# Optimization experiments

Measured on AMD Instinct MI355X. Metric: run time of the kernel, lower is better.

The kernel has to match this reference:

```python
import jax, jax.numpy as jnp
import numpy as np

N_NEIGHBORS = 9
MIN_STD, MAX_STD = 0.01, 0.5
EPS_NORM = 1e-8


def setup_inputs() -> dict:
    key = jax.random.key(0)
    k1, k2, k3 = jax.random.split(key, 3)
    B, C, H, W = 8, 1024, 28, 28
    M, D = 16384, 1024
    features = jax.random.normal(k1, (B, C, H, W), dtype=jnp.float32)
    memory_bank = jax.random.normal(k2, (M, D), dtype=jnp.float32)
    influence_weight = jnp.ones((D,), dtype=jnp.float32)
    distance_weight = jnp.ones((1,), dtype=jnp.float32)
    eps = jax.random.normal(k3, (B * H * W, D), dtype=jnp.float32)  # randn_like noise
    return {"features": features, "memory_bank": memory_bank,
            "influence_weight": influence_weight, "distance_weight": distance_weight,
            "eps": eps}


def reference(features, memory_bank, influence_weight, distance_weight, eps):
    B, C, H, W = features.shape
    M, D = memory_bank.shape
    x = features.transpose(0, 2, 3, 1).reshape(B * H * W, C)  # [N, D]
    N = x.shape[0]

    d2 = (jnp.sum(x * x, axis=1, keepdims=True)
          + jnp.sum(memory_bank * memory_bank, axis=1)[None, :]
          - 2.0 * (x @ memory_bank.T))  # [N, M]
    dist = jnp.sqrt(jnp.clip(d2, 1e-12))

    k = min(N_NEIGHBORS, M)
    neg_topd, idx = jax.lax.top_k(-dist, k)  # smallest-k distances
    topk_distances = -neg_topd  # [N, k]

    # Per-dimension influence: mean |x - nn| over k neighbors, scaled by weight
    nn_feats = memory_bank[idx]  # [N, k, D] gather
    influence = jnp.abs(x[:, None, :] - nn_feats).mean(axis=1) * influence_weight[None, :]  # [N, D]

    # Row-wise normalization (torch std is unbiased, ddof=1)
    infl_norm = ((influence - influence.mean(axis=-1, keepdims=True))
                 / (jnp.std(influence, axis=-1, ddof=1, keepdims=True) + EPS_NORM))

    # Distance signal: per-row mean distance, normalized by global stats of the
    # [N, D]-expanded tensor (each row value repeated D times -> same mean,
    # unbiased std uses N*D - 1 in the denominator).
    ds = topk_distances.mean(axis=-1, keepdims=True)  # [N, 1]
    full_mean = ds.mean()
    full_std = jnp.sqrt(jnp.sum((ds - full_mean) ** 2) * D / (N * D - 1))
    dist_norm = (ds - full_mean) / (full_std + EPS_NORM)  # [N, 1], broadcasts over D

    combined = infl_norm + distance_weight * dist_norm  # [N, D]
    noise_std = MIN_STD + (MAX_STD - MIN_STD) * jax.nn.sigmoid(combined)

    noised = (x + eps * noise_std).reshape(B, H, W, C).transpose(0, 3, 1, 2)
    influence_map = influence.mean(axis=-1).reshape(B, H, W)
    noise_std_map = noise_std.mean(axis=-1).reshape(B, H, W)
    return noised, influence_map, noise_std_map
```

## Files before the change

kernel.cpp:

```cpp
#include <hip/hip_runtime.h>
#include <hip/hip_bf16.h>
#include <stdint.h>

#define N_ROWS 6272
#define DIM    1024
#define M_ROWS 16384
#define KNN    9
#define BMS    128
#define BNS    128
#define NPANEL 128
#define TOPC   6
#define NCAND  (NPANEL * 2 * TOPC)
#define TRR    16

typedef __attribute__((ext_vector_type(4))) float f32x4;
typedef __attribute__((ext_vector_type(4))) int   i32x4;
typedef __attribute__((ext_vector_type(16))) int  i32x16;

#define QSCALE 31.75f

__device__ __forceinline__ void async16(const void* g, void* l) {
  __builtin_amdgcn_global_load_lds(
      (const __attribute__((address_space(1))) unsigned int*)g,
      (__attribute__((address_space(3))) unsigned int*)l, 16, 0, 0);
}

__device__ __forceinline__ int quant8(float v) {
  return __float2int_rn(fminf(fmaxf(v, -4.f), 4.f) * QSCALE);
}

__device__ __forceinline__ int kswz(int row, int col) {
  return col ^ ((row & 7) << 2) ^ (((row >> 3) & 1) << 5);
}

__global__ void k_prep_x(const float* __restrict__ feat,
                         float* __restrict__ xf, signed char* __restrict__ xq) {
  const int n = blockIdx.x;
  const int b = n / 784, hw = n % 784;
  const float* src = feat + (size_t)b * (1024 * 784) + hw;
  float* xrow = xf + (size_t)n * DIM;
  signed char* qrow = xq + (size_t)n * DIM;
  for (int c = threadIdx.x; c < DIM; c += 256) {
    float v = src[(size_t)c * 784];
    xrow[c] = v;
    qrow[c] = (signed char)quant8(v);
  }
}

__global__ void k_prep_m(const float* __restrict__ mb,
                         signed char* __restrict__ mq, int* __restrict__ mni) {
  const int j = blockIdx.x;
  const int t = threadIdx.x;
  const float* src = mb + (size_t)j * DIM;
  signed char* dst = mq + (size_t)j * DIM;
  int s = 0;
  for (int c = t; c < DIM; c += 256) {
    const int q = quant8(src[c]);
    dst[c] = (signed char)q;
    s += q * q;
  }
  __shared__ int red[4];
#pragma unroll
  for (int o = 32; o >= 1; o >>= 1) s += __shfl_down(s, o);
  if ((t & 63) == 0) red[t >> 6] = s;
  __syncthreads();
  if (t == 0) mni[j] = red[0] + red[1] + red[2] + red[3];
}

__launch_bounds__(256, 2)
__global__ void k_score(const signed char* __restrict__ xq,
                        const signed char* __restrict__ mq,
                        const int* __restrict__ mni,
                        unsigned int* __restrict__ cand, int jhalf) {
  __shared__ signed char S[65536];
  __shared__ int mns[BNS];
  int* Kbuf = (int*)S;

  const int bx = blockIdx.x;
  const int xcd = bx & 7, i = bx >> 3;
  const int panel = i & 7, agroup = i >> 3;
  const int j0 = jhalf * 8192 + xcd * 1024 + panel * BNS;
  const int pglob = jhalf * 64 + xcd * 8 + panel;

  const int t = threadIdx.x;
  const int lane = t & 63, w = t >> 6;
  const int wr = w >> 1, wc = w & 1;
  const int l31 = lane & 31, kh = lane >> 5;

  int offL[4], aOff[4];
  const signed char* bP[4];
#pragma unroll
  for (int cpy = 0; cpy < 4; ++cpy) {
    const int off = cpy * 4096 + t * 16;
    const int row = off >> 7;
    const int col = (off & 127) ^ ((row & 7) << 4);
    offL[cpy] = off;
    aOff[cpy] = row * DIM + col;
    bP[cpy] = mq + (size_t)(j0 + row) * DIM + col;
  }
  if (t < BNS) mns[t] = mni[j0 + t];

#pragma unroll 1
  for (int k7 = 0; k7 < 7; ++k7) {
    const int tile = agroup + 7 * k7;
    const int r0 = tile * BMS;
    const signed char* aT = xq + (size_t)r0 * DIM;

    i32x16 acc[2][2];
#pragma unroll
    for (int mi = 0; mi < 2; ++mi)
#pragma unroll
      for (int ni = 0; ni < 2; ++ni)
#pragma unroll
        for (int r = 0; r < 16; ++r) acc[mi][ni][r] = 0;

#pragma unroll
    for (int cpy = 0; cpy < 4; ++cpy) {
      async16(aT + aOff[cpy], S + offL[cpy]);
      async16(bP[cpy], S + 32768 + offL[cpy]);
    }
#pragma unroll 1
    for (int kt = 0; kt < 8; ++kt) {
      if (kt < 7) {
        const int kk = (kt + 1) * 128;
        const int nb = ((kt + 1) & 1) * 16384;
#pragma unroll
        for (int cpy = 0; cpy < 4; ++cpy) {
          async16(aT + aOff[cpy] + kk, S + nb + offL[cpy]);
          async16(bP[cpy] + kk, S + 32768 + nb + offL[cpy]);
        }
        asm volatile("s_waitcnt vmcnt(8)" ::: "memory");
      } else {
        asm volatile("s_waitcnt vmcnt(0)" ::: "memory");
      }
      __builtin_amdgcn_s_barrier();
      const signed char* Ab = S + (kt & 1) * 16384;
      const signed char* Bb = S + 32768 + (kt & 1) * 16384;
      __builtin_amdgcn_s_setprio(1);
#pragma unroll
      for (int ks = 0; ks < 4; ++ks) {
        const int kcol = ks * 32 + kh * 16;
        i32x4 a[2], b[2];
#pragma unroll
        for (int mi = 0; mi < 2; ++mi) {
          const int row = wr * 64 + mi * 32 + l31;
          a[mi] = *(const i32x4*)(Ab + row * 128 + (kcol ^ ((row & 7) << 4)));
        }
#pragma unroll
        for (int ni = 0; ni < 2; ++ni) {
          const int row = wc * 64 + ni * 32 + l31;
          b[ni] = *(const i32x4*)(Bb + row * 128 + (kcol ^ ((row & 7) << 4)));
        }
#pragma unroll
        for (int mi = 0; mi < 2; ++mi)
#pragma unroll
          for (int ni = 0; ni < 2; ++ni)
            acc[mi][ni] = __builtin_amdgcn_mfma_i32_32x32x32_i8(a[mi], b[ni], acc[mi][ni], 0, 0, 0);
      }
      __builtin_amdgcn_s_setprio(0);
      asm volatile("" ::: "memory");
      __builtin_amdgcn_s_barrier();
    }

#pragma unroll
    for (int mi = 0; mi < 2; ++mi)
#pragma unroll
      for (int ni = 0; ni < 2; ++ni) {
        const int col = wc * 64 + ni * 32 + l31;
        const int mn = mns[col];
#pragma unroll
        for (int r = 0; r < 16; ++r) {
          const int row = wr * 64 + mi * 32 + 4 * kh + (r & 3) + 8 * (r >> 2);
          Kbuf[row * 128 + kswz(row, col)] = mn - 2 * acc[mi][ni][r];
        }
      }
    __syncthreads();
    {
      const int row = t >> 1, half = t & 1;
      unsigned tk[TOPC];
#pragma unroll
      for (int s = 0; s < TOPC; ++s) tk[s] = 0xFFFFFFFFu;
#pragma unroll
      for (int q = 0; q < 16; ++q) {
        const int cl = half * 64 + q * 4;
        const i32x4 v = *(const i32x4*)(Kbuf + row * 128 + kswz(row, cl));
#pragma unroll
        for (int e = 0; e < 4; ++e) {
          const unsigned p = (((unsigned)(v[e] + (1 << 25)) >> 11) << 14)
                             | (unsigned)(j0 + cl + e);
          if (p < tk[0]) {
            tk[0] = p;
#pragma unroll
            for (int s = 0; s < TOPC - 1; ++s) {
              const unsigned hi = tk[s] > tk[s + 1] ? tk[s] : tk[s + 1];
              const unsigned lo = tk[s] > tk[s + 1] ? tk[s + 1] : tk[s];
              tk[s] = hi; tk[s + 1] = lo;
            }
          }
        }
      }
      const size_t base = (size_t)(r0 + row) * NCAND + (size_t)(pglob * 2 + half) * TOPC;
#pragma unroll
      for (int s = 0; s < TOPC; ++s) cand[base + s] = tk[s];
    }
    __syncthreads();
  }
}

__global__ void k_rerank(const float* __restrict__ xf, const float* __restrict__ mb,
                         const unsigned int* __restrict__ cand,
                         int* __restrict__ idx9, double* __restrict__ dsv) {
  const int n = blockIdx.x, t = threadIdx.x;
  __shared__ float    xs[DIM];
  __shared__ unsigned cs[NCAND];
  __shared__ unsigned sel[TRR];
  __shared__ double dpart[256];
  __shared__ double d2s[TRR];
  __shared__ double dist_s[TRR];
  __shared__ int    rank_s[TRR];

  const float* xrow = xf + (size_t)n * DIM;
  for (int c = t; c < DIM; c += 256) xs[c] = xrow[c];
  const size_t cb = (size_t)n * NCAND;
  for (int s = t; s < NCAND; s += 256) cs[s] = cand[cb + s];
  __syncthreads();

  if (t < 64) {
    unsigned ck[24];
#pragma unroll
    for (int s = 0; s < 24; ++s) ck[s] = cs[t + 64 * s];
    for (int it = 0; it < TRR; ++it) {
      unsigned best = ck[0];
#pragma unroll
      for (int s = 1; s < 24; ++s) best = best < ck[s] ? best : ck[s];
#pragma unroll
      for (int off = 32; off >= 1; off >>= 1) {
        const unsigned o = (unsigned)__shfl_xor((int)best, off);
        best = best < o ? best : o;
      }
      if (t == 0) sel[it] = best;
#pragma unroll
      for (int s = 0; s < 24; ++s) if (ck[s] == best) ck[s] = 0xFFFFFFFFu;
    }
  }
  __syncthreads();
  {
    const int s = t >> 4, l16 = t & 15;
    const int j = (int)(sel[s] & 16383u);
    const float* mrow = mb + (size_t)j * DIM;
    double a = 0.0;
    for (int i = 0; i < 64; ++i) {
      const int c = l16 + (i << 4);
      const double d = (double)xs[c] - (double)mrow[c];
      a += d * d;
    }
    dpart[t] = a;
  }
  __syncthreads();
  if (t < TRR) {
    double v = 0.0;
    for (int i = 0; i < 16; ++i) v += dpart[t * 16 + i];
    d2s[t] = v;
    dist_s[t] = sqrt(v < 1e-12 ? 1e-12 : v);
  }
  __syncthreads();
  if (t < TRR) {
    const double v = d2s[t]; const int id = (int)(sel[t] & 16383u);
    int r = 0;
    for (int u = 0; u < TRR; ++u) {
      const double vu = d2s[u];
      const int idu = (int)(sel[u] & 16383u);
      if (vu < v || (vu == v && idu < id)) ++r;
    }
    rank_s[t] = r;
    if (r < KNN) idx9[n * KNN + r] = id;
  }
  __syncthreads();
  if (t == 0) {
    double sum = 0.0;
    for (int u = 0; u < TRR; ++u) if (rank_s[u] < KNN) sum += dist_s[u];
    dsv[n] = sum * (1.0 / KNN);
  }
}

__global__ void k_dsstats(const double* __restrict__ dsv, double* __restrict__ stats) {
  __shared__ double red[1024];
  const int t = threadIdx.x;
  double s = 0.0;
  for (int i = t; i < N_ROWS; i += 1024) s += dsv[i];
  red[t] = s; __syncthreads();
  for (int o = 512; o >= 1; o >>= 1) { if (t < o) red[t] += red[t + o]; __syncthreads(); }
  const double mean = red[0] / (double)N_ROWS;
  __syncthreads();
  double v = 0.0;
  for (int i = t; i < N_ROWS; i += 1024) { const double d = dsv[i] - mean; v += d * d; }
  red[t] = v; __syncthreads();
  for (int o = 512; o >= 1; o >>= 1) { if (t < o) red[t] += red[t + o]; __syncthreads(); }
  if (t == 0) {
    const double fullstd = sqrt(red[0] * (double)DIM / ((double)N_ROWS * DIM - 1.0));
    stats[0] = mean;
    stats[1] = fullstd + 1e-8;
  }
}

__global__ void k_final(const float* __restrict__ xf, const float* __restrict__ mb,
                        const float* __restrict__ iw, const float* __restrict__ dwp,
                        const float* __restrict__ eps, const int* __restrict__ idx9,
                        const double* __restrict__ dsv, const double* __restrict__ stats,
                        float* __restrict__ out) {
  const int n = blockIdx.x, t = threadIdx.x;
  __shared__ float xs[DIM];
  __shared__ int js[KNN];
  __shared__ float rs1[4], rs2[4];
  const float* xrow = xf + (size_t)n * DIM;
  for (int c = t; c < DIM; c += 256) xs[c] = xrow[c];
  if (t < KNN) js[t] = idx9[n * KNN + t];
  __syncthreads();

  float infl[4];
  float s1 = 0.f, s2 = 0.f;
#pragma unroll
  for (int q = 0; q < 4; ++q) {
    const int c = t + q * 256;
    const float x = xs[c];
    float a = 0.f;
#pragma unroll
    for (int k = 0; k < KNN; ++k) a += fabsf(x - mb[(size_t)js[k] * DIM + c]);
    const float v = a * (1.0f / KNN) * iw[c];
    infl[q] = v; s1 += v; s2 += v * v;
  }
#pragma unroll
  for (int o = 32; o >= 1; o >>= 1) { s1 += __shfl_down(s1, o); s2 += __shfl_down(s2, o); }
  if ((t & 63) == 0) { rs1[t >> 6] = s1; rs2[t >> 6] = s2; }
  __syncthreads();
  const float sum = rs1[0] + rs1[1] + rs1[2] + rs1[3];
  const float sq  = rs2[0] + rs2[1] + rs2[2] + rs2[3];
  const float mean = sum * (1.0f / DIM);
  float var = (sq - (float)DIM * mean * mean) * (1.0f / (DIM - 1));
  var = fmaxf(var, 0.f);
  const float inv = 1.0f / (sqrtf(var) + 1e-8f);
  const float dn = (float)(((double)dsv[n] - stats[0]) / stats[1]);
  const float zb = dwp[0] * dn;

  const int b = n / 784, hw = n % 784;
  float* op = out + (size_t)b * (1024 * 784) + hw;
  const float* ep = eps + (size_t)n * DIM;
  float si = 0.f, sn = 0.f;
#pragma unroll
  for (int q = 0; q < 4; ++q) {
    const int c = t + q * 256;
    const float v = infl[q];
    const float z = (v - mean) * inv + zb;
    const float ns = 0.01f + 0.49f / (1.0f + expf(-z));
    op[(size_t)c * 784] = xs[c] + ep[c] * ns;
    si += v; sn += ns;
  }
  __syncthreads();
#pragma unroll
  for (int o = 32; o >= 1; o >>= 1) { si += __shfl_down(si, o); sn += __shfl_down(sn, o); }
  if ((t & 63) == 0) { rs1[t >> 6] = si; rs2[t >> 6] = sn; }
  __syncthreads();
  if (t == 0) {
    out[6422528 + n]        = (rs1[0] + rs1[1] + rs1[2] + rs1[3]) * (1.0f / DIM);
    out[6422528 + 6272 + n] = (rs2[0] + rs2[1] + rs2[2] + rs2[3]) * (1.0f / DIM);
  }
}

extern "C" void kernel_launch(void* const* d_in, const int* in_sizes, int n_in,
                              void* d_out, int out_size, void* d_ws, size_t ws_size,
                              hipStream_t stream) {
  (void)in_sizes; (void)n_in; (void)out_size; (void)ws_size;
  const float* feat = (const float*)d_in[0];
  const float* mb   = (const float*)d_in[1];
  const float* iw   = (const float*)d_in[2];
  const float* dw   = (const float*)d_in[3];
  const float* eps  = (const float*)d_in[4];
  float* out = (float*)d_out;

  char* p = (char*)d_ws;
  float* xf = (float*)p;                     p += (size_t)N_ROWS * DIM * 4;
  signed char* xq = (signed char*)p;         p += (size_t)N_ROWS * DIM;
  signed char* mq = (signed char*)p;         p += (size_t)M_ROWS * DIM;
  int* mni = (int*)p;                        p += (size_t)M_ROWS * 4;
  unsigned int* cand = (unsigned int*)p;     p += (size_t)N_ROWS * NCAND * 4;
  int* idx9 = (int*)p;                       p += (size_t)N_ROWS * KNN * 4;
  p = (char*)(((uintptr_t)p + 255) & ~(uintptr_t)255);
  double* dsv = (double*)p;                  p += (size_t)N_ROWS * 8;
  double* stats = (double*)p;                p += 64;

  k_prep_x<<<N_ROWS, 256, 0, stream>>>(feat, xf, xq);
  k_prep_m<<<M_ROWS, 256, 0, stream>>>(mb, mq, mni);
  k_score<<<448, 256, 0, stream>>>(xq, mq, mni, cand, 0);
  k_score<<<448, 256, 0, stream>>>(xq, mq, mni, cand, 1);
  k_rerank<<<N_ROWS, 256, 0, stream>>>(xf, mb, cand, idx9, dsv);
  k_dsstats<<<1, 1024, 0, stream>>>(dsv, stats);
  k_final<<<N_ROWS, 256, 0, stream>>>(xf, mb, iw, dw, eps, idx9, dsv, stats, out);
}
```

Baseline: 425.7 us.

## Tile transposes, merge score launches, register-staged LDS loads, atomic stats

The input transpose in prep_x now uses 32x32 shared-memory tiles so both the global reads and writes are coalesced. The final output transpose moves to a new tiled kernel that reads from a row-major scratch buffer reusing cand. The two k_score launches are merged into one 512-block grid with 16 panels per XCD. The async global-to-LDS copies are replaced by register-staged loads into padded LDS rows (stride 160) with a different swizzle. The separate dsstats kernel is removed in favour of double atomicAdds of sum and sum-of-squares in rerank, which adds atomic contention and a less numerically stable variance formula.

```diff
diff --git a/kernel.cpp b/kernel.cpp
--- a/kernel.cpp
+++ b/kernel.cpp
@@ -12,6 +12,7 @@
 #define TOPC   6
 #define NCAND  (NPANEL * 2 * TOPC)
 #define TRR    16
+#define LSTR   160
 
 typedef __attribute__((ext_vector_type(4))) float f32x4;
 typedef __attribute__((ext_vector_type(4))) int   i32x4;
@@ -19,12 +20,6 @@
 
 #define QSCALE 31.75f
 
-__device__ __forceinline__ void async16(const void* g, void* l) {
-  __builtin_amdgcn_global_load_lds(
-      (const __attribute__((address_space(1))) unsigned int*)g,
-      (__attribute__((address_space(3))) unsigned int*)l, 16, 0, 0);
-}
-
 __device__ __forceinline__ int quant8(float v) {
   return __float2int_rn(fminf(fmaxf(v, -4.f), 4.f) * QSCALE);
 }
@@ -34,16 +29,29 @@
 }
 
 __global__ void k_prep_x(const float* __restrict__ feat,
-                         float* __restrict__ xf, signed char* __restrict__ xq) {
-  const int n = blockIdx.x;
-  const int b = n / 784, hw = n % 784;
-  const float* src = feat + (size_t)b * (1024 * 784) + hw;
-  float* xrow = xf + (size_t)n * DIM;
-  signed char* qrow = xq + (size_t)n * DIM;
-  for (int c = threadIdx.x; c < DIM; c += 256) {
-    float v = src[(size_t)c * 784];
-    xrow[c] = v;
-    qrow[c] = (signed char)quant8(v);
+                         float* __restrict__ xf, signed char* __restrict__ xq,
+                         double* __restrict__ stats) {
+  if (blockIdx.x == 0 && threadIdx.x < 2) stats[threadIdx.x] = 0.0;
+  __shared__ float tile[32][33];
+  const int ct = blockIdx.x & 31, nt = blockIdx.x >> 5;
+  const int c0 = ct * 32, n0 = nt * 32;
+  const int tx = threadIdx.x & 31, ty = threadIdx.x >> 5;
+  {
+    const int n = n0 + tx;
+    const int b = n / 784, hw = n % 784;
+    const float* src = feat + (size_t)b * 802816 + hw;
+#pragma unroll
+    for (int q = 0; q < 4; ++q)
+      tile[ty + q * 8][tx] = src[(size_t)(c0 + ty + q * 8) * 784];
+  }
+  __syncthreads();
+#pragma unroll
+  for (int q = 0; q < 4; ++q) {
+    const int nn = n0 + ty + q * 8;
+    const int cc = c0 + tx;
+    const float v = tile[tx][ty + q * 8];
+    xf[(size_t)nn * DIM + cc] = v;
+    xq[(size_t)nn * DIM + cc] = (signed char)quant8(v);
   }
 }
 
@@ -71,40 +79,41 @@
 __global__ void k_score(const signed char* __restrict__ xq,
                         const signed char* __restrict__ mq,
                         const int* __restrict__ mni,
-                        unsigned int* __restrict__ cand, int jhalf) {
-  __shared__ signed char S[65536];
-  __shared__ int mns[BNS];
+                        unsigned int* __restrict__ cand) {
+  __shared__ signed char S[81920];
   int* Kbuf = (int*)S;
 
   const int bx = blockIdx.x;
   const int xcd = bx & 7, i = bx >> 3;
-  const int panel = i & 7, agroup = i >> 3;
-  const int j0 = jhalf * 8192 + xcd * 1024 + panel * BNS;
-  const int pglob = jhalf * 64 + xcd * 8 + panel;
+  const int panel = i & 15, agroup = i >> 4;
+  const int j0 = xcd * 2048 + panel * BNS;
+  const int pglob = xcd * 16 + panel;
 
   const int t = threadIdx.x;
   const int lane = t & 63, w = t >> 6;
   const int wr = w >> 1, wc = w & 1;
   const int l31 = lane & 31, kh = lane >> 5;
 
-  int offL[4], aOff[4];
-  const signed char* bP[4];
+  int srcOff[4], ldsOff[4];
 #pragma unroll
   for (int cpy = 0; cpy < 4; ++cpy) {
-    const int off = cpy * 4096 + t * 16;
-    const int row = off >> 7;
-    const int col = (off & 127) ^ ((row & 7) << 4);
-    offL[cpy] = off;
-    aOff[cpy] = row * DIM + col;
-    bP[cpy] = mq + (size_t)(j0 + row) * DIM + col;
-  }
-  if (t < BNS) mns[t] = mni[j0 + t];
-
+    const int c = cpy * 256 + t;
+    const int row = c >> 3, s = c & 7;
+    srcOff[cpy] = row * DIM + s * 16;
+    ldsOff[cpy] = row * LSTR + ((s ^ (row & 7)) << 4);
+  }
+  const signed char* bBase = mq + (size_t)j0 * DIM;
+
+  int mn_[2];
+#pragma unroll
+  for (int ni = 0; ni < 2; ++ni) mn_[ni] = mni[j0 + wc * 64 + ni * 32 + l31];
+
+  const int tcount = (agroup == 0) ? 13 : 12;
 #pragma unroll 1
-  for (int k7 = 0; k7 < 7; ++k7) {
-    const int tile = agroup + 7 * k7;
+  for (int k7 = 0; k7 < tcount; ++k7) {
+    const int tile = agroup + 4 * k7;
     const int r0 = tile * BMS;
-    const signed char* aT = xq + (size_t)r0 * DIM;
+    const signed char* aBase = xq + (size_t)r0 * DIM;
 
     i32x16 acc[2][2];
 #pragma unroll
@@ -114,42 +123,47 @@
 #pragma unroll
         for (int r = 0; r < 16; ++r) acc[mi][ni][r] = 0;
 
+    i32x4 ra[4], rb[4];
 #pragma unroll
     for (int cpy = 0; cpy < 4; ++cpy) {
-      async16(aT + aOff[cpy], S + offL[cpy]);
-      async16(bP[cpy], S + 32768 + offL[cpy]);
-    }
+      ra[cpy] = *(const i32x4*)(aBase + srcOff[cpy]);
+      rb[cpy] = *(const i32x4*)(bBase + srcOff[cpy]);
+    }
+#pragma unroll
+    for (int cpy = 0; cpy < 4; ++cpy) {
+      *(i32x4*)(S + ldsOff[cpy]) = ra[cpy];
+      *(i32x4*)(S + 40960 + ldsOff[cpy]) = rb[cpy];
+    }
+    asm volatile("s_waitcnt lgkmcnt(0)" ::: "memory");
+    __builtin_amdgcn_s_barrier();
+
 #pragma unroll 1
     for (int kt = 0; kt < 8; ++kt) {
+      const int cb = (kt & 1) * 20480;
+      const signed char* Ab = S + cb;
+      const signed char* Bb = S + 40960 + cb;
       if (kt < 7) {
         const int kk = (kt + 1) * 128;
-        const int nb = ((kt + 1) & 1) * 16384;
 #pragma unroll
         for (int cpy = 0; cpy < 4; ++cpy) {
-          async16(aT + aOff[cpy] + kk, S + nb + offL[cpy]);
-          async16(bP[cpy] + kk, S + 32768 + nb + offL[cpy]);
-        }
-        asm volatile("s_waitcnt vmcnt(8)" ::: "memory");
-      } else {
-        asm volatile("s_waitcnt vmcnt(0)" ::: "memory");
-      }
-      __builtin_amdgcn_s_barrier();
-      const signed char* Ab = S + (kt & 1) * 16384;
-      const signed char* Bb = S + 32768 + (kt & 1) * 16384;
+          ra[cpy] = *(const i32x4*)(aBase + srcOff[cpy] + kk);
+          rb[cpy] = *(const i32x4*)(bBase + srcOff[cpy] + kk);
+        }
+      }
       __builtin_amdgcn_s_setprio(1);
 #pragma unroll
       for (int ks = 0; ks < 4; ++ks) {
-        const int kcol = ks * 32 + kh * 16;
+        const int sr = 2 * ks + kh;
         i32x4 a[2], b[2];
 #pragma unroll
         for (int mi = 0; mi < 2; ++mi) {
-          const int row = wr * 64 + mi * 32 + l31;
-          a[mi] = *(const i32x4*)(Ab + row * 128 + (kcol ^ ((row & 7) << 4)));
+          const int r = wr * 64 + mi * 32 + l31;
+          a[mi] = *(const i32x4*)(Ab + r * LSTR + ((sr ^ (r & 7)) << 4));
         }
 #pragma unroll
         for (int ni = 0; ni < 2; ++ni) {
-          const int row = wc * 64 + ni * 32 + l31;
-          b[ni] = *(const i32x4*)(Bb + row * 128 + (kcol ^ ((row & 7) << 4)));
+          const int r = wc * 64 + ni * 32 + l31;
+          b[ni] = *(const i32x4*)(Bb + r * LSTR + ((sr ^ (r & 7)) << 4));
         }
 #pragma unroll
         for (int mi = 0; mi < 2; ++mi)
@@ -158,7 +172,15 @@
             acc[mi][ni] = __builtin_amdgcn_mfma_i32_32x32x32_i8(a[mi], b[ni], acc[mi][ni], 0, 0, 0);
       }
       __builtin_amdgcn_s_setprio(0);
-      asm volatile("" ::: "memory");
+      if (kt < 7) {
+        const int nb = ((kt + 1) & 1) * 20480;
+#pragma unroll
+        for (int cpy = 0; cpy < 4; ++cpy) {
+          *(i32x4*)(S + nb + ldsOff[cpy]) = ra[cpy];
+          *(i32x4*)(S + 40960 + nb + ldsOff[cpy]) = rb[cpy];
+        }
+      }
+      asm volatile("s_waitcnt lgkmcnt(0)" ::: "memory");
       __builtin_amdgcn_s_barrier();
     }
 
@@ -167,7 +189,7 @@
 #pragma unroll
       for (int ni = 0; ni < 2; ++ni) {
         const int col = wc * 64 + ni * 32 + l31;
-        const int mn = mns[col];
+        const int mn = mn_[ni];
 #pragma unroll
         for (int r = 0; r < 16; ++r) {
           const int row = wr * 64 + mi * 32 + 4 * kh + (r & 3) + 8 * (r >> 2);
@@ -209,7 +231,8 @@
 
 __global__ void k_rerank(const float* __restrict__ xf, const float* __restrict__ mb,
                          const unsigned int* __restrict__ cand,
-                         int* __restrict__ idx9, double* __restrict__ dsv) {
+                         int* __restrict__ idx9, double* __restrict__ dsv,
+                         double* __restrict__ stats) {
   const int n = blockIdx.x, t = threadIdx.x;
   __shared__ float    xs[DIM];
   __shared__ unsigned cs[NCAND];
@@ -279,35 +302,18 @@
   if (t == 0) {
     double sum = 0.0;
     for (int u = 0; u < TRR; ++u) if (rank_s[u] < KNN) sum += dist_s[u];
-    dsv[n] = sum * (1.0 / KNN);
-  }
-}
-
-__global__ void k_dsstats(const double* __restrict__ dsv, double* __restrict__ stats) {
-  __shared__ double red[1024];
-  const int t = threadIdx.x;
-  double s = 0.0;
-  for (int i = t; i < N_ROWS; i += 1024) s += dsv[i];
-  red[t] = s; __syncthreads();
-  for (int o = 512; o >= 1; o >>= 1) { if (t < o) red[t] += red[t + o]; __syncthreads(); }
-  const double mean = red[0] / (double)N_ROWS;
-  __syncthreads();
-  double v = 0.0;
-  for (int i = t; i < N_ROWS; i += 1024) { const double d = dsv[i] - mean; v += d * d; }
-  red[t] = v; __syncthreads();
-  for (int o = 512; o >= 1; o >>= 1) { if (t < o) red[t] += red[t + o]; __syncthreads(); }
-  if (t == 0) {
-    const double fullstd = sqrt(red[0] * (double)DIM / ((double)N_ROWS * DIM - 1.0));
-    stats[0] = mean;
-    stats[1] = fullstd + 1e-8;
-  }
-}
-
-__global__ void k_final(const float* __restrict__ xf, const float* __restrict__ mb,
-                        const float* __restrict__ iw, const float* __restrict__ dwp,
-                        const float* __restrict__ eps, const int* __restrict__ idx9,
-                        const double* __restrict__ dsv, const double* __restrict__ stats,
-                        float* __restrict__ out) {
+    const double m9 = sum * (1.0 / KNN);
+    dsv[n] = m9;
+    atomicAdd(&stats[0], m9);
+    atomicAdd(&stats[1], m9 * m9);
+  }
+}
+
+__global__ void k_final_b(const float* __restrict__ xf, const float* __restrict__ mb,
+                          const float* __restrict__ iw, const float* __restrict__ dwp,
+                          const float* __restrict__ eps, const int* __restrict__ idx9,
+                          const double* __restrict__ dsv, const double* __restrict__ stats,
+                          float* __restrict__ tn, float* __restrict__ out) {
   const int n = blockIdx.x, t = threadIdx.x;
   __shared__ float xs[DIM];
   __shared__ int js[KNN];
@@ -339,11 +345,16 @@
   float var = (sq - (float)DIM * mean * mean) * (1.0f / (DIM - 1));
   var = fmaxf(var, 0.f);
   const float inv = 1.0f / (sqrtf(var) + 1e-8f);
-  const float dn = (float)(((double)dsv[n] - stats[0]) / stats[1]);
+
+  const double S1 = stats[0], S2 = stats[1];
+  const double meanD = S1 / (double)N_ROWS;
+  double varTop = S2 - S1 * S1 / (double)N_ROWS;
+  if (varTop < 0.0) varTop = 0.0;
+  const double fullstd = sqrt(varTop * (double)DIM / ((double)N_ROWS * DIM - 1.0)) + 1e-8;
+  const float dn = (float)((dsv[n] - meanD) / fullstd);
   const float zb = dwp[0] * dn;
 
-  const int b = n / 784, hw = n % 784;
-  float* op = out + (size_t)b * (1024 * 784) + hw;
+  float* trow = tn + (size_t)n * DIM;
   const float* ep = eps + (size_t)n * DIM;
   float si = 0.f, sn = 0.f;
 #pragma unroll
@@ -352,7 +363,7 @@
     const float v = infl[q];
     const float z = (v - mean) * inv + zb;
     const float ns = 0.01f + 0.49f / (1.0f + expf(-z));
-    op[(size_t)c * 784] = xs[c] + ep[c] * ns;
+    trow[c] = xs[c] + ep[c] * ns;
     si += v; sn += ns;
   }
   __syncthreads();
@@ -364,6 +375,23 @@
     out[6422528 + n]        = (rs1[0] + rs1[1] + rs1[2] + rs1[3]) * (1.0f / DIM);
     out[6422528 + 6272 + n] = (rs2[0] + rs2[1] + rs2[2] + rs2[3]) * (1.0f / DIM);
   }
+}
+
+__global__ void k_tr(const float* __restrict__ tn, float* __restrict__ out) {
+  __shared__ float tile[32][33];
+  const int ct = blockIdx.x & 31, nt = blockIdx.x >> 5;
+  const int c0 = ct * 32, n0 = nt * 32;
+  const int tx = threadIdx.x & 31, ty = threadIdx.x >> 5;
+#pragma unroll
+  for (int q = 0; q < 4; ++q)
+    tile[ty + q * 8][tx] = tn[(size_t)(n0 + ty + q * 8) * DIM + c0 + tx];
+  __syncthreads();
+  const int n = n0 + tx;
+  const int b = n / 784, hw = n % 784;
+  float* dst = out + (size_t)b * 802816 + hw;
+#pragma unroll
+  for (int q = 0; q < 4; ++q)
+    dst[(size_t)(c0 + ty + q * 8) * 784] = tile[tx][ty + q * 8];
 }
 
 extern "C" void kernel_launch(void* const* d_in, const int* in_sizes, int n_in,
@@ -387,12 +415,12 @@
   p = (char*)(((uintptr_t)p + 255) & ~(uintptr_t)255);
   double* dsv = (double*)p;                  p += (size_t)N_ROWS * 8;
   double* stats = (double*)p;                p += 64;
-
-  k_prep_x<<<N_ROWS, 256, 0, stream>>>(feat, xf, xq);
+  float* tn = (float*)cand;
+
+  k_prep_x<<<6272, 256, 0, stream>>>(feat, xf, xq, stats);
   k_prep_m<<<M_ROWS, 256, 0, stream>>>(mb, mq, mni);
-  k_score<<<448, 256, 0, stream>>>(xq, mq, mni, cand, 0);
-  k_score<<<448, 256, 0, stream>>>(xq, mq, mni, cand, 1);
-  k_rerank<<<N_ROWS, 256, 0, stream>>>(xf, mb, cand, idx9, dsv);
-  k_dsstats<<<1, 1024, 0, stream>>>(dsv, stats);
-  k_final<<<N_ROWS, 256, 0, stream>>>(xf, mb, iw, dw, eps, idx9, dsv, stats, out);
-}
+  k_score<<<512, 256, 0, stream>>>(xq, mq, mni, cand);
+  k_rerank<<<N_ROWS, 256, 0, stream>>>(xf, mb, cand, idx9, dsv, stats);
+  k_final_b<<<N_ROWS, 256, 0, stream>>>(xf, mb, iw, dw, eps, idx9, dsv, stats, tn, out);
+  k_tr<<<6272, 256, 0, stream>>>(tn, out);
+}
```

New measurement: 435.4 us. +2.3%, slower.
